# Kernel tuning notes

Measured on AMD Instinct MI355X. Metric: run time of the kernel, lower is better.

## Reference

```python
import jax, jax.numpy as jnp
import numpy as np

N = 100000
E = 1600000
FEAT = 128
EMBED = 128
CLASSES = 40


def _sage_conv(x, src, dst, W_l, W_r, b, n_nodes):
    # PyG SAGEConv (mean aggr): out = mean_{j in N(i)} x_j @ W_l + x_i @ W_r + b
    msg = x[src]                                                  # [E, d] gather
    agg = jax.ops.segment_sum(msg, dst, num_segments=n_nodes)     # [N, d]
    cnt = jax.ops.segment_sum(jnp.ones((src.shape[0], 1), x.dtype), dst,
                              num_segments=n_nodes)               # [N, 1]
    agg = agg / jnp.maximum(cnt, 1.0)                             # mean (0 for isolated)
    return agg @ W_l + x @ W_r + b


def setup_inputs() -> dict:
    key = jax.random.key(0)
    ks = jax.random.split(key, 10)
    s = lambda d: 1.0 / np.sqrt(d)
    x = jax.random.normal(ks[0], (N, FEAT), dtype=jnp.float32)
    edge_index = jax.random.randint(ks[1], (2, E), 0, N, dtype=jnp.int64)
    W1_l = jax.random.uniform(ks[2], (FEAT, EMBED), jnp.float32, -s(FEAT), s(FEAT))
    W1_r = jax.random.uniform(ks[3], (FEAT, EMBED), jnp.float32, -s(FEAT), s(FEAT))
    b1 = jnp.zeros((EMBED,), jnp.float32)
    W2_l = jax.random.uniform(ks[4], (EMBED, EMBED), jnp.float32, -s(EMBED), s(EMBED))
    W2_r = jax.random.uniform(ks[5], (EMBED, EMBED), jnp.float32, -s(EMBED), s(EMBED))
    b2 = jnp.zeros((EMBED,), jnp.float32)
    W_out = jax.random.uniform(ks[6], (EMBED, CLASSES), jnp.float32, -s(EMBED), s(EMBED))
    b_out = jax.random.uniform(ks[7], (CLASSES,), jnp.float32, -s(EMBED), s(EMBED))
    return {"x": x, "edge_index": edge_index,
            "W1_l": W1_l, "W1_r": W1_r, "b1": b1,
            "W2_l": W2_l, "W2_r": W2_r, "b2": b2,
            "W_out": W_out, "b_out": b_out}


def reference(x, edge_index, W1_l, W1_r, b1, W2_l, W2_r, b2, W_out, b_out):
    src, dst = edge_index[0], edge_index[1]
    n = x.shape[0]
    h = _sage_conv(x, src, dst, W1_l, W1_r, b1, n)   # [N, EMBED]
    h = _sage_conv(h, src, dst, W2_l, W2_r, b2, n)   # [N, EMBED]
    g = jnp.mean(h, axis=0, keepdims=True)           # global_mean_pool, batch=None -> [1, EMBED]
    return g @ W_out + b_out                          # [1, CLASSES]
```

## Files before the change

### kernel.cpp

```cpp
#include <hip/hip_runtime.h>


#define NN    100000
#define NE    1600000
#define FEAT  128
#define NCLS  40
#define NR    16
#define RSIZE 6250
#define NC    16
#define PER   (NE / 4 / NC)
#define FSB   2048


__global__ __launch_bounds__(1024) void k_cnt16(const int4* __restrict__ dst4, int* __restrict__ partial) {
    __shared__ int tab[RSIZE];
    const int c = blockIdx.x, r = blockIdx.y;
    for (int j = threadIdx.x; j < RSIZE; j += 1024) tab[j] = 0;
    __syncthreads();
    const int base = r * RSIZE;
    const int i0 = c * PER;
    for (int i = i0 + (int)threadIdx.x; i < i0 + PER; i += 1024) {
        int4 d = dst4[i];
        unsigned a;
        a = (unsigned)(d.x - base); if (a < RSIZE) atomicAdd(&tab[a], 1);
        a = (unsigned)(d.y - base); if (a < RSIZE) atomicAdd(&tab[a], 1);
        a = (unsigned)(d.z - base); if (a < RSIZE) atomicAdd(&tab[a], 1);
        a = (unsigned)(d.w - base); if (a < RSIZE) atomicAdd(&tab[a], 1);
    }
    __syncthreads();
    int* out = partial + (size_t)(r * NC + c) * RSIZE;
    for (int j = threadIdx.x; j < RSIZE; j += 1024) out[j] = tab[j];
}

__global__ __launch_bounds__(1024) void k_scat16(const int4* __restrict__ src4, const int4* __restrict__ dst4,
                                                 const float* __restrict__ val, float* __restrict__ partial) {
    __shared__ float tab[RSIZE];
    const int c = blockIdx.x, r = blockIdx.y;
    for (int j = threadIdx.x; j < RSIZE; j += 1024) tab[j] = 0.f;
    __syncthreads();
    const int base = r * RSIZE;
    const int i0 = c * PER;
    for (int i = i0 + (int)threadIdx.x; i < i0 + PER; i += 1024) {
        int4 s = src4[i];
        int4 d = dst4[i];
        unsigned a;
        a = (unsigned)(s.x - base); if (a < RSIZE) atomicAdd(&tab[a], val[d.x]);
        a = (unsigned)(s.y - base); if (a < RSIZE) atomicAdd(&tab[a], val[d.y]);
        a = (unsigned)(s.z - base); if (a < RSIZE) atomicAdd(&tab[a], val[d.z]);
        a = (unsigned)(s.w - base); if (a < RSIZE) atomicAdd(&tab[a], val[d.w]);
    }
    __syncthreads();
    float* out = partial + (size_t)(r * NC + c) * RSIZE;
    for (int j = threadIdx.x; j < RSIZE; j += 1024) out[j] = tab[j];
}

__global__ __launch_bounds__(256) void k_merge_invc(const int* __restrict__ partial, float* __restrict__ invc) {
    int i = blockIdx.x * 256 + threadIdx.x;
    if (i >= NN) return;
    int r = i / RSIZE, j = i - r * RSIZE;
    const int* p = partial + (size_t)r * NC * RSIZE + j;
    int cn = 0;
    #pragma unroll
    for (int c = 0; c < NC; ++c) cn += p[(size_t)c * RSIZE];
    invc[i] = 1.0f / (float)(cn > 0 ? cn : 1);
}

__global__ __launch_bounds__(256) void k_merge_ws(const float* __restrict__ partial, const float* __restrict__ invc,
                                                  float* __restrict__ ws, float* __restrict__ u) {
    int i = blockIdx.x * 256 + threadIdx.x;
    if (i >= NN) return;
    int r = i / RSIZE, j = i - r * RSIZE;
    const float* p = partial + (size_t)r * NC * RSIZE + j;
    float w = 0.f;
    #pragma unroll
    for (int c = 0; c < NC; ++c) w += p[(size_t)c * RSIZE];
    ws[i] = w;
    u[i] = w * invc[i];
}

__global__ __launch_bounds__(256) void k_merge_t(const float* __restrict__ partial, float* __restrict__ t) {
    int i = blockIdx.x * 256 + threadIdx.x;
    if (i >= NN) return;
    int r = i / RSIZE, j = i - r * RSIZE;
    const float* p = partial + (size_t)r * NC * RSIZE + j;
    float v = 0.f;
    #pragma unroll
    for (int c = 0; c < NC; ++c) v += p[(size_t)c * RSIZE];
    t[i] = v;
}


__global__ __launch_bounds__(256) void k_fs1(const float* __restrict__ x,
                                             const float* __restrict__ ws,
                                             const float* __restrict__ t,
                                             float* __restrict__ p1) {
    int lane = threadIdx.x & 31;
    int grp  = threadIdx.x >> 5;
    int row0 = blockIdx.x * 8 + grp;
    const int rstride = FSB * 8;

    float sx0=0,sx1=0,sx2=0,sx3=0;
    float sw0=0,sw1=0,sw2=0,sw3=0;
    float st0=0,st1=0,st2=0,st3=0;
    float wsum = 0.f;

    for (int r = row0; r < NN; r += rstride) {
        const float4* xr = (const float4*)(x + (size_t)r * FEAT);
        float4 v = xr[lane];
        float wr = ws[r];
        float tr = t[r];
        sx0 += v.x; sx1 += v.y; sx2 += v.z; sx3 += v.w;
        sw0 += wr*v.x; sw1 += wr*v.y; sw2 += wr*v.z; sw3 += wr*v.w;
        st0 += tr*v.x; st1 += tr*v.y; st2 += tr*v.z; st3 += tr*v.w;
        if (lane == 0) wsum += wr;
    }

    __shared__ float shx[8][32][4];
    __shared__ float shw[8][32][4];
    __shared__ float sht[8][32][4];
    __shared__ float shwsum[8];
    shx[grp][lane][0]=sx0; shx[grp][lane][1]=sx1; shx[grp][lane][2]=sx2; shx[grp][lane][3]=sx3;
    shw[grp][lane][0]=sw0; shw[grp][lane][1]=sw1; shw[grp][lane][2]=sw2; shw[grp][lane][3]=sw3;
    sht[grp][lane][0]=st0; sht[grp][lane][1]=st1; sht[grp][lane][2]=st2; sht[grp][lane][3]=st3;
    if (lane == 0) shwsum[grp] = wsum;
    __syncthreads();

    if (grp == 0) {
        const int b = blockIdx.x;
        float ax[4], aw[4], at[4];
        #pragma unroll
        for (int c = 0; c < 4; ++c) { ax[c]=shx[0][lane][c]; aw[c]=shw[0][lane][c]; at[c]=sht[0][lane][c]; }
        #pragma unroll
        for (int g = 1; g < 8; ++g) {
            #pragma unroll
            for (int c = 0; c < 4; ++c) {
                ax[c]+=shx[g][lane][c]; aw[c]+=shw[g][lane][c]; at[c]+=sht[g][lane][c];
            }
        }
        #pragma unroll
        for (int c = 0; c < 4; ++c) {
            p1[(size_t)(        4*lane + c) * FSB + b] = ax[c];
            p1[(size_t)(FEAT  + 4*lane + c) * FSB + b] = aw[c];
            p1[(size_t)(2*FEAT+ 4*lane + c) * FSB + b] = at[c];
        }
        if (lane == 0) {
            float w = shwsum[0];
            #pragma unroll
            for (int g = 1; g < 8; ++g) w += shwsum[g];
            p1[(size_t)(3*FEAT) * FSB + b] = w;
        }
    }
}

__global__ __launch_bounds__(256) void k_fs2(const float* __restrict__ p1, float* __restrict__ sums) {
    const int v = blockIdx.x;
    float s = 0.f;
    for (int b = threadIdx.x; b < FSB; b += 256) s += p1[(size_t)v * FSB + b];
    __shared__ float sh[256];
    sh[threadIdx.x] = s;
    __syncthreads();
    for (int off = 128; off > 0; off >>= 1) {
        if (threadIdx.x < off) sh[threadIdx.x] += sh[threadIdx.x + off];
        __syncthreads();
    }
    if (threadIdx.x == 0) sums[v] = sh[0];
}


__global__ __launch_bounds__(256) void k_count_dev(const int4* __restrict__ dst4, int* __restrict__ cnt) {
    int i = blockIdx.x * 256 + threadIdx.x;
    if (i >= NE / 4) return;
    int4 d = dst4[i];
    atomicAdd(&cnt[d.x], 1); atomicAdd(&cnt[d.y], 1);
    atomicAdd(&cnt[d.z], 1); atomicAdd(&cnt[d.w], 1);
}

__global__ __launch_bounds__(256) void k_inv_dev(const int* __restrict__ cnt, float* __restrict__ invc) {
    int i = blockIdx.x * 256 + threadIdx.x;
    if (i >= NN) return;
    int c = cnt[i];
    invc[i] = 1.0f / (float)(c > 0 ? c : 1);
}

__global__ __launch_bounds__(256) void k_ws_dev(const int4* __restrict__ src4, const int4* __restrict__ dst4,
                                                const float* __restrict__ invc, float* __restrict__ ws) {
    int i = blockIdx.x * 256 + threadIdx.x;
    if (i >= NE / 4) return;
    int4 s = src4[i];
    int4 d = dst4[i];
    atomicAdd(&ws[s.x], invc[d.x]); atomicAdd(&ws[s.y], invc[d.y]);
    atomicAdd(&ws[s.z], invc[d.z]); atomicAdd(&ws[s.w], invc[d.w]);
}

__global__ __launch_bounds__(256) void k_u_dev(const float* __restrict__ ws, const float* __restrict__ invc,
                                               float* __restrict__ u) {
    int i = blockIdx.x * 256 + threadIdx.x;
    if (i >= NN) return;
    u[i] = ws[i] * invc[i];
}

__global__ __launch_bounds__(256) void k_t_dev(const int4* __restrict__ src4, const int4* __restrict__ dst4,
                                               const float* __restrict__ u, float* __restrict__ t) {
    int i = blockIdx.x * 256 + threadIdx.x;
    if (i >= NE / 4) return;
    int4 s = src4[i];
    int4 d = dst4[i];
    atomicAdd(&t[s.x], u[d.x]); atomicAdd(&t[s.y], u[d.y]);
    atomicAdd(&t[s.z], u[d.z]); atomicAdd(&t[s.w], u[d.w]);
}

__global__ __launch_bounds__(256) void k_fs_atom(const float* __restrict__ x,
                                                 const float* __restrict__ ws,
                                                 const float* __restrict__ t,
                                                 float* __restrict__ sums) {
    int lane = threadIdx.x & 31;
    int grp  = threadIdx.x >> 5;
    int row0 = blockIdx.x * 8 + grp;
    int rstride = gridDim.x * 8;
    float sx0=0,sx1=0,sx2=0,sx3=0, sw0=0,sw1=0,sw2=0,sw3=0, st0=0,st1=0,st2=0,st3=0, wsum=0.f;
    for (int r = row0; r < NN; r += rstride) {
        const float4* xr = (const float4*)(x + (size_t)r * FEAT);
        float4 v = xr[lane];
        float wr = ws[r], tr = t[r];
        sx0+=v.x; sx1+=v.y; sx2+=v.z; sx3+=v.w;
        sw0+=wr*v.x; sw1+=wr*v.y; sw2+=wr*v.z; sw3+=wr*v.w;
        st0+=tr*v.x; st1+=tr*v.y; st2+=tr*v.z; st3+=tr*v.w;
        if (lane==0) wsum += wr;
    }
    __shared__ float shx[8][32][4], shw[8][32][4], sht[8][32][4], shwsum[8];
    shx[grp][lane][0]=sx0; shx[grp][lane][1]=sx1; shx[grp][lane][2]=sx2; shx[grp][lane][3]=sx3;
    shw[grp][lane][0]=sw0; shw[grp][lane][1]=sw1; shw[grp][lane][2]=sw2; shw[grp][lane][3]=sw3;
    sht[grp][lane][0]=st0; sht[grp][lane][1]=st1; sht[grp][lane][2]=st2; sht[grp][lane][3]=st3;
    if (lane==0) shwsum[grp]=wsum;
    __syncthreads();
    if (grp==0) {
        float ax[4], aw[4], at[4];
        #pragma unroll
        for (int c=0;c<4;++c){ax[c]=shx[0][lane][c];aw[c]=shw[0][lane][c];at[c]=sht[0][lane][c];}
        #pragma unroll
        for (int g=1;g<8;++g)
            #pragma unroll
            for (int c=0;c<4;++c){ax[c]+=shx[g][lane][c];aw[c]+=shw[g][lane][c];at[c]+=sht[g][lane][c];}
        #pragma unroll
        for (int c=0;c<4;++c){
            atomicAdd(&sums[        4*lane+c], ax[c]);
            atomicAdd(&sums[FEAT  + 4*lane+c], aw[c]);
            atomicAdd(&sums[2*FEAT+ 4*lane+c], at[c]);
        }
        if (lane==0){
            float w=shwsum[0];
            #pragma unroll
            for (int g=1;g<8;++g) w+=shwsum[g];
            atomicAdd(&sums[3*FEAT], w);
        }
    }
}


__global__ __launch_bounds__(128) void k_final(const float* __restrict__ sums,
                                               const float* __restrict__ W1l, const float* __restrict__ W1r,
                                               const float* __restrict__ b1,
                                               const float* __restrict__ W2l, const float* __restrict__ W2r,
                                               const float* __restrict__ b2,
                                               const float* __restrict__ Wout, const float* __restrict__ bout,
                                               float* __restrict__ out) {
    __shared__ float Sx[FEAT], Sw[FEAT], St[FEAT], M1[FEAT], S2[FEAT], G[FEAT];
    __shared__ float Wsum;
    int f = threadIdx.x;
    Sx[f] = sums[f];
    Sw[f] = sums[FEAT + f];
    St[f] = sums[2*FEAT + f];
    if (f == 0) Wsum = sums[3*FEAT];
    __syncthreads();

    float m1 = (float)NN * b1[f];
    float s2 = Wsum * b1[f];
    for (int k = 0; k < FEAT; ++k) {
        float wl = W1l[k*FEAT + f];
        float wr = W1r[k*FEAT + f];
        m1 += Sw[k]*wl + Sx[k]*wr;
        s2 += St[k]*wl + Sw[k]*wr;
    }
    M1[f] = m1; S2[f] = s2;
    __syncthreads();

    float g = 0.f;
    for (int k = 0; k < FEAT; ++k)
        g += S2[k]*W2l[k*FEAT + f] + M1[k]*W2r[k*FEAT + f];
    g = g * (1.0f/(float)NN) + b2[f];
    G[f] = g;
    __syncthreads();

    if (f < NCLS) {
        float o = bout[f];
        for (int k = 0; k < FEAT; ++k)
            o += G[k]*Wout[k*NCLS + f];
        out[f] = o;
    }
}


extern "C" void kernel_launch(void* const* d_in, const int* in_sizes, int n_in,
                              void* d_out, int out_size, void* d_ws, size_t ws_size,
                              hipStream_t stream) {
    const float* x    = (const float*)d_in[0];
    const int*   ei   = (const int*)d_in[1];
    const float* W1l  = (const float*)d_in[2];
    const float* W1r  = (const float*)d_in[3];
    const float* b1   = (const float*)d_in[4];
    const float* W2l  = (const float*)d_in[5];
    const float* W2r  = (const float*)d_in[6];
    const float* b2   = (const float*)d_in[7];
    const float* Wout = (const float*)d_in[8];
    const float* bout = (const float*)d_in[9];
    float* out = (float*)d_out;

    const int4* src4 = (const int4*)ei;
    const int4* dst4 = (const int4*)(ei + NE);

    const size_t need_lds = ((size_t)NR * NC * RSIZE + 640 + (size_t)4 * NN) * 4;

    if (ws_size >= need_lds) {
        float* partial = (float*)d_ws;
        size_t po = (size_t)NR * NC * RSIZE;
        float* sums = (float*)d_ws + po;
        float* invc = (float*)d_ws + po + 640;
        float* ws   = (float*)d_ws + po + 640 + (size_t)NN;
        float* u    = (float*)d_ws + po + 640 + (size_t)2*NN;
        float* t    = (float*)d_ws + po + 640 + (size_t)3*NN;
        float* p1   = partial;

        dim3 eg(NC, NR);
        const int NB = (NN + 255) / 256;

        k_cnt16<<<eg, 1024, 0, stream>>>(dst4, (int*)partial);
        k_merge_invc<<<NB, 256, 0, stream>>>((const int*)partial, invc);
        k_scat16<<<eg, 1024, 0, stream>>>(src4, dst4, invc, partial);
        k_merge_ws<<<NB, 256, 0, stream>>>(partial, invc, ws, u);
        k_scat16<<<eg, 1024, 0, stream>>>(src4, dst4, u, partial);
        k_merge_t<<<NB, 256, 0, stream>>>(partial, t);
        k_fs1<<<FSB, 256, 0, stream>>>(x, ws, t, p1);
        k_fs2<<<385, 256, 0, stream>>>(p1, sums);
        k_final<<<1, 128, 0, stream>>>(sums, W1l, W1r, b1, W2l, W2r, b2, Wout, bout, out);
    } else {
        int*   cnt  = (int*)d_ws;
        float* wsv  = (float*)d_ws + NN;
        float* t    = (float*)d_ws + 2*NN;
        float* sums = (float*)d_ws + 3*NN;
        float* invc = (float*)d_ws + 3*NN + 640;
        float* u    = (float*)d_ws + 3*NN + 640 + NN;

        hipMemsetAsync(d_ws, 0, ((size_t)3*NN + 640) * 4, stream);

        const int EB4 = (NE/4 + 255) / 256;
        const int NB  = (NN + 255) / 256;
        k_count_dev<<<EB4, 256, 0, stream>>>(dst4, cnt);
        k_inv_dev<<<NB, 256, 0, stream>>>(cnt, invc);
        k_ws_dev<<<EB4, 256, 0, stream>>>(src4, dst4, invc, wsv);
        k_u_dev<<<NB, 256, 0, stream>>>(wsv, invc, u);
        k_t_dev<<<EB4, 256, 0, stream>>>(src4, dst4, u, t);
        k_fs_atom<<<256, 256, 0, stream>>>(x, wsv, t, sums);
        k_final<<<1, 128, 0, stream>>>(sums, W1l, W1r, b1, W2l, W2r, b2, Wout, bout, out);
    }
}
```

Measured before the change: 205.7 us.

## Pack degree counts as 16-bit pairs and widen LDS range partitions

The degree-count histogram now packs two 16-bit counters per 32-bit LDS word, so each block covers twice as many nodes and fewer range passes over the edge list are needed. The scatter kernels use larger LDS tables (14336 floats) with 7 range slices and 64 edge chunks instead of 16x16, which cuts redundant re-reads of the edge arrays and raises the block count. The 16-bit counters assume no per-chunk count overflows 65535, and the larger partial buffers add merge traffic and need more workspace.

```diff
diff --git a/kernel.cpp b/kernel.cpp
--- a/kernel.cpp
+++ b/kernel.cpp
@@ -5,87 +5,106 @@
 #define NE    1600000
 #define FEAT  128
 #define NCLS  40
-#define NR    16
-#define RSIZE 6250
-#define NC    16
-#define PER   (NE / 4 / NC)
 #define FSB   2048
 
-
-__global__ __launch_bounds__(1024) void k_cnt16(const int4* __restrict__ dst4, int* __restrict__ partial) {
-    __shared__ int tab[RSIZE];
+#define B_RS   14336
+#define B_NR   7
+#define B_RSC  28672
+#define B_NRC  4
+#define B_NC   64
+
+#define S_RS   6250
+#define S_NR   16
+#define S_RSC  12500
+#define S_NRC  8
+#define S_NC   16
+
+
+template<int RSC, int NRC, int NCv>
+__global__ __launch_bounds__(1024) void k_cnt_p(const int4* __restrict__ dst4,
+                                                unsigned* __restrict__ partial) {
+    __shared__ unsigned tab[RSC / 2];
     const int c = blockIdx.x, r = blockIdx.y;
-    for (int j = threadIdx.x; j < RSIZE; j += 1024) tab[j] = 0;
-    __syncthreads();
-    const int base = r * RSIZE;
-    const int i0 = c * PER;
-    for (int i = i0 + (int)threadIdx.x; i < i0 + PER; i += 1024) {
+    for (int j = threadIdx.x; j < RSC / 2; j += 1024) tab[j] = 0u;
+    __syncthreads();
+    const int base = r * RSC;
+    const int PERv = (NE / 4) / NCv;
+    const int i0 = c * PERv;
+    for (int i = i0 + (int)threadIdx.x; i < i0 + PERv; i += 1024) {
         int4 d = dst4[i];
         unsigned a;
-        a = (unsigned)(d.x - base); if (a < RSIZE) atomicAdd(&tab[a], 1);
-        a = (unsigned)(d.y - base); if (a < RSIZE) atomicAdd(&tab[a], 1);
-        a = (unsigned)(d.z - base); if (a < RSIZE) atomicAdd(&tab[a], 1);
-        a = (unsigned)(d.w - base); if (a < RSIZE) atomicAdd(&tab[a], 1);
-    }
-    __syncthreads();
-    int* out = partial + (size_t)(r * NC + c) * RSIZE;
-    for (int j = threadIdx.x; j < RSIZE; j += 1024) out[j] = tab[j];
-}
-
-__global__ __launch_bounds__(1024) void k_scat16(const int4* __restrict__ src4, const int4* __restrict__ dst4,
-                                                 const float* __restrict__ val, float* __restrict__ partial) {
-    __shared__ float tab[RSIZE];
+        a = (unsigned)(d.x - base); if (a < RSC) atomicAdd(&tab[a >> 1], 1u << ((a & 1) * 16));
+        a = (unsigned)(d.y - base); if (a < RSC) atomicAdd(&tab[a >> 1], 1u << ((a & 1) * 16));
+        a = (unsigned)(d.z - base); if (a < RSC) atomicAdd(&tab[a >> 1], 1u << ((a & 1) * 16));
+        a = (unsigned)(d.w - base); if (a < RSC) atomicAdd(&tab[a >> 1], 1u << ((a & 1) * 16));
+    }
+    __syncthreads();
+    unsigned* out = partial + (size_t)(r * NCv + c) * (RSC / 2);
+    for (int j = threadIdx.x; j < RSC / 2; j += 1024) out[j] = tab[j];
+}
+
+template<int RS, int NRv, int NCv>
+__global__ __launch_bounds__(1024) void k_scat(const int4* __restrict__ src4, const int4* __restrict__ dst4,
+                                               const float* __restrict__ val, float* __restrict__ partial) {
+    __shared__ float tab[RS];
     const int c = blockIdx.x, r = blockIdx.y;
-    for (int j = threadIdx.x; j < RSIZE; j += 1024) tab[j] = 0.f;
-    __syncthreads();
-    const int base = r * RSIZE;
-    const int i0 = c * PER;
-    for (int i = i0 + (int)threadIdx.x; i < i0 + PER; i += 1024) {
+    for (int j = threadIdx.x; j < RS; j += 1024) tab[j] = 0.f;
+    __syncthreads();
+    const int base = r * RS;
+    const int PERv = (NE / 4) / NCv;
+    const int i0 = c * PERv;
+    for (int i = i0 + (int)threadIdx.x; i < i0 + PERv; i += 1024) {
         int4 s = src4[i];
         int4 d = dst4[i];
         unsigned a;
-        a = (unsigned)(s.x - base); if (a < RSIZE) atomicAdd(&tab[a], val[d.x]);
-        a = (unsigned)(s.y - base); if (a < RSIZE) atomicAdd(&tab[a], val[d.y]);
-        a = (unsigned)(s.z - base); if (a < RSIZE) atomicAdd(&tab[a], val[d.z]);
-        a = (unsigned)(s.w - base); if (a < RSIZE) atomicAdd(&tab[a], val[d.w]);
-    }
-    __syncthreads();
-    float* out = partial + (size_t)(r * NC + c) * RSIZE;
-    for (int j = threadIdx.x; j < RSIZE; j += 1024) out[j] = tab[j];
-}
-
-__global__ __launch_bounds__(256) void k_merge_invc(const int* __restrict__ partial, float* __restrict__ invc) {
+        a = (unsigned)(s.x - base); if (a < RS) atomicAdd(&tab[a], val[d.x]);
+        a = (unsigned)(s.y - base); if (a < RS) atomicAdd(&tab[a], val[d.y]);
+        a = (unsigned)(s.z - base); if (a < RS) atomicAdd(&tab[a], val[d.z]);
+        a = (unsigned)(s.w - base); if (a < RS) atomicAdd(&tab[a], val[d.w]);
+    }
+    __syncthreads();
+    float* out = partial + (size_t)(r * NCv + c) * RS;
+    for (int j = threadIdx.x; j < RS; j += 1024) out[j] = tab[j];
+}
+
+template<int RSC, int NRC, int NCv>
+__global__ __launch_bounds__(256) void k_merge_invc(const unsigned* __restrict__ partial,
+                                                    float* __restrict__ invc) {
     int i = blockIdx.x * 256 + threadIdx.x;
     if (i >= NN) return;
-    int r = i / RSIZE, j = i - r * RSIZE;
-    const int* p = partial + (size_t)r * NC * RSIZE + j;
+    int r = i / RSC, j = i - r * RSC;
+    const unsigned* p = partial + (size_t)r * NCv * (RSC / 2) + (j >> 1);
+    const unsigned sh = (unsigned)(j & 1) * 16u;
     int cn = 0;
     #pragma unroll
-    for (int c = 0; c < NC; ++c) cn += p[(size_t)c * RSIZE];
+    for (int c = 0; c < NCv; ++c) cn += (int)((p[(size_t)c * (RSC / 2)] >> sh) & 0xFFFFu);
     invc[i] = 1.0f / (float)(cn > 0 ? cn : 1);
 }
 
-__global__ __launch_bounds__(256) void k_merge_ws(const float* __restrict__ partial, const float* __restrict__ invc,
+template<int RS, int NRv, int NCv>
+__global__ __launch_bounds__(256) void k_merge_ws(const float* __restrict__ partial,
+                                                  const float* __restrict__ invc,
                                                   float* __restrict__ ws, float* __restrict__ u) {
     int i = blockIdx.x * 256 + threadIdx.x;
     if (i >= NN) return;
-    int r = i / RSIZE, j = i - r * RSIZE;
-    const float* p = partial + (size_t)r * NC * RSIZE + j;
+    int r = i / RS, j = i - r * RS;
+    const float* p = partial + (size_t)r * NCv * RS + j;
     float w = 0.f;
     #pragma unroll
-    for (int c = 0; c < NC; ++c) w += p[(size_t)c * RSIZE];
+    for (int c = 0; c < NCv; ++c) w += p[(size_t)c * RS];
     ws[i] = w;
     u[i] = w * invc[i];
 }
 
+template<int RS, int NRv, int NCv>
 __global__ __launch_bounds__(256) void k_merge_t(const float* __restrict__ partial, float* __restrict__ t) {
     int i = blockIdx.x * 256 + threadIdx.x;
     if (i >= NN) return;
-    int r = i / RSIZE, j = i - r * RSIZE;
-    const float* p = partial + (size_t)r * NC * RSIZE + j;
+    int r = i / RS, j = i - r * RS;
+    const float* p = partial + (size_t)r * NCv * RS + j;
     float v = 0.f;
     #pragma unroll
-    for (int c = 0; c < NC; ++c) v += p[(size_t)c * RSIZE];
+    for (int c = 0; c < NCv; ++c) v += p[(size_t)c * RS];
     t[i] = v;
 }
 
@@ -300,6 +319,36 @@
 }
 
 
+template<int RS, int NRv, int RSC, int NRC, int NCv>
+static void run_cfg(const float* x, const int4* src4, const int4* dst4,
+                    const float* W1l, const float* W1r, const float* b1,
+                    const float* W2l, const float* W2r, const float* b2,
+                    const float* Wout, const float* bout,
+                    float* out, void* d_ws, hipStream_t stream) {
+    const size_t scat_par = (size_t)NRv * NCv * RS;
+    float* partial = (float*)d_ws;
+    float* sums = (float*)d_ws + scat_par;
+    float* invc = (float*)d_ws + scat_par + 640;
+    float* ws   = (float*)d_ws + scat_par + 640 + (size_t)NN;
+    float* u    = (float*)d_ws + scat_par + 640 + (size_t)2*NN;
+    float* t    = (float*)d_ws + scat_par + 640 + (size_t)3*NN;
+    float* p1   = partial;
+
+    const int NB = (NN + 255) / 256;
+    dim3 gc(NCv, NRC);
+    dim3 gs(NCv, NRv);
+
+    k_cnt_p<RSC, NRC, NCv><<<gc, 1024, 0, stream>>>(dst4, (unsigned*)partial);
+    k_merge_invc<RSC, NRC, NCv><<<NB, 256, 0, stream>>>((const unsigned*)partial, invc);
+    k_scat<RS, NRv, NCv><<<gs, 1024, 0, stream>>>(src4, dst4, invc, partial);
+    k_merge_ws<RS, NRv, NCv><<<NB, 256, 0, stream>>>(partial, invc, ws, u);
+    k_scat<RS, NRv, NCv><<<gs, 1024, 0, stream>>>(src4, dst4, u, partial);
+    k_merge_t<RS, NRv, NCv><<<NB, 256, 0, stream>>>(partial, t);
+    k_fs1<<<FSB, 256, 0, stream>>>(x, ws, t, p1);
+    k_fs2<<<385, 256, 0, stream>>>(p1, sums);
+    k_final<<<1, 128, 0, stream>>>(sums, W1l, W1r, b1, W2l, W2r, b2, Wout, bout, out);
+}
+
 extern "C" void kernel_launch(void* const* d_in, const int* in_sizes, int n_in,
                               void* d_out, int out_size, void* d_ws, size_t ws_size,
                               hipStream_t stream) {
@@ -318,30 +367,16 @@
     const int4* src4 = (const int4*)ei;
     const int4* dst4 = (const int4*)(ei + NE);
 
-    const size_t need_lds = ((size_t)NR * NC * RSIZE + 640 + (size_t)4 * NN) * 4;
-
-    if (ws_size >= need_lds) {
-        float* partial = (float*)d_ws;
-        size_t po = (size_t)NR * NC * RSIZE;
-        float* sums = (float*)d_ws + po;
-        float* invc = (float*)d_ws + po + 640;
-        float* ws   = (float*)d_ws + po + 640 + (size_t)NN;
-        float* u    = (float*)d_ws + po + 640 + (size_t)2*NN;
-        float* t    = (float*)d_ws + po + 640 + (size_t)3*NN;
-        float* p1   = partial;
-
-        dim3 eg(NC, NR);
-        const int NB = (NN + 255) / 256;
-
-        k_cnt16<<<eg, 1024, 0, stream>>>(dst4, (int*)partial);
-        k_merge_invc<<<NB, 256, 0, stream>>>((const int*)partial, invc);
-        k_scat16<<<eg, 1024, 0, stream>>>(src4, dst4, invc, partial);
-        k_merge_ws<<<NB, 256, 0, stream>>>(partial, invc, ws, u);
-        k_scat16<<<eg, 1024, 0, stream>>>(src4, dst4, u, partial);
-        k_merge_t<<<NB, 256, 0, stream>>>(partial, t);
-        k_fs1<<<FSB, 256, 0, stream>>>(x, ws, t, p1);
-        k_fs2<<<385, 256, 0, stream>>>(p1, sums);
-        k_final<<<1, 128, 0, stream>>>(sums, W1l, W1r, b1, W2l, W2r, b2, Wout, bout, out);
+    auto need = [](size_t scat_par) { return (scat_par + 640 + (size_t)4 * NN) * 4; };
+    const size_t big_par   = (size_t)B_NR * B_NC * B_RS;
+    const size_t small_par = (size_t)S_NR * S_NC * S_RS;
+
+    if (ws_size >= need(big_par)) {
+        run_cfg<B_RS, B_NR, B_RSC, B_NRC, B_NC>(x, src4, dst4, W1l, W1r, b1, W2l, W2r, b2,
+                                                Wout, bout, out, d_ws, stream);
+    } else if (ws_size >= need(small_par)) {
+        run_cfg<S_RS, S_NR, S_RSC, S_NRC, S_NC>(x, src4, dst4, W1l, W1r, b1, W2l, W2r, b2,
+                                                Wout, bout, out, d_ws, stream);
     } else {
         int*   cnt  = (int*)d_ws;
         float* wsv  = (float*)d_ws + NN;
```

Result: slower. 221.9 us (+7.9%).

## Fuse all stages into one cooperative persistent kernel with grid syncs

Applied to the files above, without the earlier changes.

Replaces nine separate kernel launches (count, merges, two scatters, feature sums, final GEMV) with a single cooperative kernel of 256 blocks of 1024 threads, using grid.sync between phases and a union of shared-memory tables. This removes per-launch overhead and inter-kernel gaps. In exchange it adds grid-wide barriers, the final reduction runs on one block only, and the path needs cooperative-launch support with every block co-resident.

```diff
diff --git a/kernel.cpp b/kernel.cpp
--- a/kernel.cpp
+++ b/kernel.cpp
@@ -1,4 +1,7 @@
 #include <hip/hip_runtime.h>
+#include <hip/hip_cooperative_groups.h>
+
+namespace cg = cooperative_groups;
 
 
 #define NN    100000
@@ -6,164 +9,223 @@
 #define FEAT  128
 #define NCLS  40
 #define NR    16
-#define RSIZE 6250
+#define RS    6250
 #define NC    16
-#define PER   (NE / 4 / NC)
-#define FSB   2048
-
-
-__global__ __launch_bounds__(1024) void k_cnt16(const int4* __restrict__ dst4, int* __restrict__ partial) {
-    __shared__ int tab[RSIZE];
-    const int c = blockIdx.x, r = blockIdx.y;
-    for (int j = threadIdx.x; j < RSIZE; j += 1024) tab[j] = 0;
-    __syncthreads();
-    const int base = r * RSIZE;
+#define PER   25000
+#define GRID  256
+#define BLK   1024
+
+struct FS {
+    float shx[32][32][4];
+    float shw[32][32][4];
+    float sht[32][32][4];
+    float wsum[32];
+};
+union SH {
+    unsigned ctab[RS];
+    float    ftab[RS];
+    FS       fs;
+    float    fin[800];
+};
+
+__global__ __launch_bounds__(BLK, 4) void k_all(
+        const float* __restrict__ x,
+        const int4* __restrict__ src4, const int4* __restrict__ dst4,
+        const float* __restrict__ W1l, const float* __restrict__ W1r, const float* __restrict__ b1,
+        const float* __restrict__ W2l, const float* __restrict__ W2r, const float* __restrict__ b2,
+        const float* __restrict__ Wout, const float* __restrict__ bout,
+        float* __restrict__ out,
+        float* __restrict__ partial, float* __restrict__ invc,
+        float* __restrict__ ws, float* __restrict__ u, float* __restrict__ t,
+        float* __restrict__ fsbuf) {
+    cg::grid_group grid = cg::this_grid();
+    __shared__ SH sh;
+
+    const int bid = blockIdx.x;
+    const int tid = threadIdx.x;
+    const int c = bid & (NC - 1);
+    const int r = bid >> 4;
+    const int base = r * RS;
     const int i0 = c * PER;
-    for (int i = i0 + (int)threadIdx.x; i < i0 + PER; i += 1024) {
+
+    for (int j = tid; j < RS; j += BLK) sh.ctab[j] = 0u;
+    __syncthreads();
+    for (int i = i0 + tid; i < i0 + PER; i += BLK) {
         int4 d = dst4[i];
         unsigned a;
-        a = (unsigned)(d.x - base); if (a < RSIZE) atomicAdd(&tab[a], 1);
-        a = (unsigned)(d.y - base); if (a < RSIZE) atomicAdd(&tab[a], 1);
-        a = (unsigned)(d.z - base); if (a < RSIZE) atomicAdd(&tab[a], 1);
-        a = (unsigned)(d.w - base); if (a < RSIZE) atomicAdd(&tab[a], 1);
-    }
-    __syncthreads();
-    int* out = partial + (size_t)(r * NC + c) * RSIZE;
-    for (int j = threadIdx.x; j < RSIZE; j += 1024) out[j] = tab[j];
-}
-
-__global__ __launch_bounds__(1024) void k_scat16(const int4* __restrict__ src4, const int4* __restrict__ dst4,
-                                                 const float* __restrict__ val, float* __restrict__ partial) {
-    __shared__ float tab[RSIZE];
-    const int c = blockIdx.x, r = blockIdx.y;
-    for (int j = threadIdx.x; j < RSIZE; j += 1024) tab[j] = 0.f;
-    __syncthreads();
-    const int base = r * RSIZE;
-    const int i0 = c * PER;
-    for (int i = i0 + (int)threadIdx.x; i < i0 + PER; i += 1024) {
+        a = (unsigned)(d.x - base); if (a < RS) atomicAdd(&sh.ctab[a], 1u);
+        a = (unsigned)(d.y - base); if (a < RS) atomicAdd(&sh.ctab[a], 1u);
+        a = (unsigned)(d.z - base); if (a < RS) atomicAdd(&sh.ctab[a], 1u);
+        a = (unsigned)(d.w - base); if (a < RS) atomicAdd(&sh.ctab[a], 1u);
+    }
+    __syncthreads();
+    {
+        unsigned* outp = (unsigned*)partial + (size_t)(r * NC + c) * RS;
+        for (int j = tid; j < RS; j += BLK) outp[j] = sh.ctab[j];
+    }
+    grid.sync();
+
+    {
+        int i = bid * BLK + tid;
+        if (i < NN) {
+            int rr = i / RS, jj = i - rr * RS;
+            const unsigned* p = (const unsigned*)partial + (size_t)rr * NC * RS + jj;
+            unsigned cn = 0;
+            #pragma unroll
+            for (int cc = 0; cc < NC; ++cc) cn += p[(size_t)cc * RS];
+            invc[i] = 1.0f / (float)(cn > 0u ? cn : 1u);
+        }
+    }
+    grid.sync();
+
+    for (int j = tid; j < RS; j += BLK) sh.ftab[j] = 0.f;
+    __syncthreads();
+    for (int i = i0 + tid; i < i0 + PER; i += BLK) {
         int4 s = src4[i];
         int4 d = dst4[i];
         unsigned a;
-        a = (unsigned)(s.x - base); if (a < RSIZE) atomicAdd(&tab[a], val[d.x]);
-        a = (unsigned)(s.y - base); if (a < RSIZE) atomicAdd(&tab[a], val[d.y]);
-        a = (unsigned)(s.z - base); if (a < RSIZE) atomicAdd(&tab[a], val[d.z]);
-        a = (unsigned)(s.w - base); if (a < RSIZE) atomicAdd(&tab[a], val[d.w]);
-    }
-    __syncthreads();
-    float* out = partial + (size_t)(r * NC + c) * RSIZE;
-    for (int j = threadIdx.x; j < RSIZE; j += 1024) out[j] = tab[j];
-}
-
-__global__ __launch_bounds__(256) void k_merge_invc(const int* __restrict__ partial, float* __restrict__ invc) {
-    int i = blockIdx.x * 256 + threadIdx.x;
-    if (i >= NN) return;
-    int r = i / RSIZE, j = i - r * RSIZE;
-    const int* p = partial + (size_t)r * NC * RSIZE + j;
-    int cn = 0;
-    #pragma unroll
-    for (int c = 0; c < NC; ++c) cn += p[(size_t)c * RSIZE];
-    invc[i] = 1.0f / (float)(cn > 0 ? cn : 1);
-}
-
-__global__ __launch_bounds__(256) void k_merge_ws(const float* __restrict__ partial, const float* __restrict__ invc,
-                                                  float* __restrict__ ws, float* __restrict__ u) {
-    int i = blockIdx.x * 256 + threadIdx.x;
-    if (i >= NN) return;
-    int r = i / RSIZE, j = i - r * RSIZE;
-    const float* p = partial + (size_t)r * NC * RSIZE + j;
-    float w = 0.f;
-    #pragma unroll
-    for (int c = 0; c < NC; ++c) w += p[(size_t)c * RSIZE];
-    ws[i] = w;
-    u[i] = w * invc[i];
-}
-
-__global__ __launch_bounds__(256) void k_merge_t(const float* __restrict__ partial, float* __restrict__ t) {
-    int i = blockIdx.x * 256 + threadIdx.x;
-    if (i >= NN) return;
-    int r = i / RSIZE, j = i - r * RSIZE;
-    const float* p = partial + (size_t)r * NC * RSIZE + j;
-    float v = 0.f;
-    #pragma unroll
-    for (int c = 0; c < NC; ++c) v += p[(size_t)c * RSIZE];
-    t[i] = v;
-}
-
-
-__global__ __launch_bounds__(256) void k_fs1(const float* __restrict__ x,
-                                             const float* __restrict__ ws,
-                                             const float* __restrict__ t,
-                                             float* __restrict__ p1) {
-    int lane = threadIdx.x & 31;
-    int grp  = threadIdx.x >> 5;
-    int row0 = blockIdx.x * 8 + grp;
-    const int rstride = FSB * 8;
-
-    float sx0=0,sx1=0,sx2=0,sx3=0;
-    float sw0=0,sw1=0,sw2=0,sw3=0;
-    float st0=0,st1=0,st2=0,st3=0;
-    float wsum = 0.f;
-
-    for (int r = row0; r < NN; r += rstride) {
-        const float4* xr = (const float4*)(x + (size_t)r * FEAT);
-        float4 v = xr[lane];
-        float wr = ws[r];
-        float tr = t[r];
-        sx0 += v.x; sx1 += v.y; sx2 += v.z; sx3 += v.w;
-        sw0 += wr*v.x; sw1 += wr*v.y; sw2 += wr*v.z; sw3 += wr*v.w;
-        st0 += tr*v.x; st1 += tr*v.y; st2 += tr*v.z; st3 += tr*v.w;
-        if (lane == 0) wsum += wr;
-    }
-
-    __shared__ float shx[8][32][4];
-    __shared__ float shw[8][32][4];
-    __shared__ float sht[8][32][4];
-    __shared__ float shwsum[8];
-    shx[grp][lane][0]=sx0; shx[grp][lane][1]=sx1; shx[grp][lane][2]=sx2; shx[grp][lane][3]=sx3;
-    shw[grp][lane][0]=sw0; shw[grp][lane][1]=sw1; shw[grp][lane][2]=sw2; shw[grp][lane][3]=sw3;
-    sht[grp][lane][0]=st0; sht[grp][lane][1]=st1; sht[grp][lane][2]=st2; sht[grp][lane][3]=st3;
-    if (lane == 0) shwsum[grp] = wsum;
-    __syncthreads();
-
-    if (grp == 0) {
-        const int b = blockIdx.x;
-        float ax[4], aw[4], at[4];
-        #pragma unroll
-        for (int c = 0; c < 4; ++c) { ax[c]=shx[0][lane][c]; aw[c]=shw[0][lane][c]; at[c]=sht[0][lane][c]; }
-        #pragma unroll
-        for (int g = 1; g < 8; ++g) {
-            #pragma unroll
-            for (int c = 0; c < 4; ++c) {
-                ax[c]+=shx[g][lane][c]; aw[c]+=shw[g][lane][c]; at[c]+=sht[g][lane][c];
+        a = (unsigned)(s.x - base); if (a < RS) atomicAdd(&sh.ftab[a], invc[d.x]);
+        a = (unsigned)(s.y - base); if (a < RS) atomicAdd(&sh.ftab[a], invc[d.y]);
+        a = (unsigned)(s.z - base); if (a < RS) atomicAdd(&sh.ftab[a], invc[d.z]);
+        a = (unsigned)(s.w - base); if (a < RS) atomicAdd(&sh.ftab[a], invc[d.w]);
+    }
+    __syncthreads();
+    {
+        float* outp = partial + (size_t)(r * NC + c) * RS;
+        for (int j = tid; j < RS; j += BLK) outp[j] = sh.ftab[j];
+    }
+    grid.sync();
+
+    {
+        int i = bid * BLK + tid;
+        if (i < NN) {
+            int rr = i / RS, jj = i - rr * RS;
+            const float* p = partial + (size_t)rr * NC * RS + jj;
+            float w = 0.f;
+            #pragma unroll
+            for (int cc = 0; cc < NC; ++cc) w += p[(size_t)cc * RS];
+            ws[i] = w;
+            u[i] = w * invc[i];
+        }
+    }
+    grid.sync();
+
+    for (int j = tid; j < RS; j += BLK) sh.ftab[j] = 0.f;
+    __syncthreads();
+    for (int i = i0 + tid; i < i0 + PER; i += BLK) {
+        int4 s = src4[i];
+        int4 d = dst4[i];
+        unsigned a;
+        a = (unsigned)(s.x - base); if (a < RS) atomicAdd(&sh.ftab[a], u[d.x]);
+        a = (unsigned)(s.y - base); if (a < RS) atomicAdd(&sh.ftab[a], u[d.y]);
+        a = (unsigned)(s.z - base); if (a < RS) atomicAdd(&sh.ftab[a], u[d.z]);
+        a = (unsigned)(s.w - base); if (a < RS) atomicAdd(&sh.ftab[a], u[d.w]);
+    }
+    __syncthreads();
+    {
+        float* outp = partial + (size_t)(r * NC + c) * RS;
+        for (int j = tid; j < RS; j += BLK) outp[j] = sh.ftab[j];
+    }
+    grid.sync();
+
+    {
+        int i = bid * BLK + tid;
+        if (i < NN) {
+            int rr = i / RS, jj = i - rr * RS;
+            const float* p = partial + (size_t)rr * NC * RS + jj;
+            float v = 0.f;
+            #pragma unroll
+            for (int cc = 0; cc < NC; ++cc) v += p[(size_t)cc * RS];
+            t[i] = v;
+        }
+    }
+    grid.sync();
+
+    {
+        const int lane = tid & 31;
+        const int grp  = tid >> 5;
+        float sx0=0,sx1=0,sx2=0,sx3=0;
+        float sw0=0,sw1=0,sw2=0,sw3=0;
+        float st0=0,st1=0,st2=0,st3=0;
+        float wsum = 0.f;
+        for (int row = bid * 32 + grp; row < NN; row += GRID * 32) {
+            const float4* xr = (const float4*)(x + (size_t)row * FEAT);
+            float4 v = xr[lane];
+            float wr = ws[row];
+            float tr = t[row];
+            sx0 += v.x; sx1 += v.y; sx2 += v.z; sx3 += v.w;
+            sw0 += wr*v.x; sw1 += wr*v.y; sw2 += wr*v.z; sw3 += wr*v.w;
+            st0 += tr*v.x; st1 += tr*v.y; st2 += tr*v.z; st3 += tr*v.w;
+            if (lane == 0) wsum += wr;
+        }
+        __syncthreads();
+        sh.fs.shx[grp][lane][0]=sx0; sh.fs.shx[grp][lane][1]=sx1;
+        sh.fs.shx[grp][lane][2]=sx2; sh.fs.shx[grp][lane][3]=sx3;
+        sh.fs.shw[grp][lane][0]=sw0; sh.fs.shw[grp][lane][1]=sw1;
+        sh.fs.shw[grp][lane][2]=sw2; sh.fs.shw[grp][lane][3]=sw3;
+        sh.fs.sht[grp][lane][0]=st0; sh.fs.sht[grp][lane][1]=st1;
+        sh.fs.sht[grp][lane][2]=st2; sh.fs.sht[grp][lane][3]=st3;
+        if (lane == 0) sh.fs.wsum[grp] = wsum;
+        __syncthreads();
+        if (grp == 0) {
+            float ax[4]={0,0,0,0}, aw[4]={0,0,0,0}, at[4]={0,0,0,0};
+            for (int g = 0; g < 32; ++g) {
+                #pragma unroll
+                for (int cc = 0; cc < 4; ++cc) {
+                    ax[cc] += sh.fs.shx[g][lane][cc];
+                    aw[cc] += sh.fs.shw[g][lane][cc];
+                    at[cc] += sh.fs.sht[g][lane][cc];
+                }
             }
-        }
-        #pragma unroll
-        for (int c = 0; c < 4; ++c) {
-            p1[(size_t)(        4*lane + c) * FSB + b] = ax[c];
-            p1[(size_t)(FEAT  + 4*lane + c) * FSB + b] = aw[c];
-            p1[(size_t)(2*FEAT+ 4*lane + c) * FSB + b] = at[c];
-        }
-        if (lane == 0) {
-            float w = shwsum[0];
-            #pragma unroll
-            for (int g = 1; g < 8; ++g) w += shwsum[g];
-            p1[(size_t)(3*FEAT) * FSB + b] = w;
-        }
-    }
-}
-
-__global__ __launch_bounds__(256) void k_fs2(const float* __restrict__ p1, float* __restrict__ sums) {
-    const int v = blockIdx.x;
-    float s = 0.f;
-    for (int b = threadIdx.x; b < FSB; b += 256) s += p1[(size_t)v * FSB + b];
-    __shared__ float sh[256];
-    sh[threadIdx.x] = s;
-    __syncthreads();
-    for (int off = 128; off > 0; off >>= 1) {
-        if (threadIdx.x < off) sh[threadIdx.x] += sh[threadIdx.x + off];
-        __syncthreads();
-    }
-    if (threadIdx.x == 0) sums[v] = sh[0];
+            #pragma unroll
+            for (int cc = 0; cc < 4; ++cc) {
+                fsbuf[(size_t)(        4*lane + cc) * GRID + bid] = ax[cc];
+                fsbuf[(size_t)(FEAT  + 4*lane + cc) * GRID + bid] = aw[cc];
+                fsbuf[(size_t)(2*FEAT+ 4*lane + cc) * GRID + bid] = at[cc];
+            }
+            if (lane == 0) {
+                float w = 0.f;
+                for (int g = 0; g < 32; ++g) w += sh.fs.wsum[g];
+                fsbuf[(size_t)(3*FEAT) * GRID + bid] = w;
+            }
+        }
+    }
+    grid.sync();
+
+    if (bid != 0) return;
+    for (int v = tid; v < 3*FEAT + 1; v += BLK) {
+        const float* pp = fsbuf + (size_t)v * GRID;
+        float s = 0.f;
+        for (int b = 0; b < GRID; ++b) s += pp[b];
+        sh.fin[v] = s;
+    }
+    __syncthreads();
+    if (tid < FEAT) {
+        float m1 = (float)NN * b1[tid];
+        float s2 = sh.fin[384] * b1[tid];
+        for (int k = 0; k < FEAT; ++k) {
+            float wl = W1l[k*FEAT + tid];
+            float wr = W1r[k*FEAT + tid];
+            m1 += sh.fin[128 + k] * wl + sh.fin[k] * wr;
+            s2 += sh.fin[256 + k] * wl + sh.fin[128 + k] * wr;
+        }
+        sh.fin[400 + tid] = m1;
+        sh.fin[528 + tid] = s2;
+    }
+    __syncthreads();
+    if (tid < FEAT) {
+        float g = 0.f;
+        for (int k = 0; k < FEAT; ++k)
+            g += sh.fin[528 + k] * W2l[k*FEAT + tid] + sh.fin[400 + k] * W2r[k*FEAT + tid];
+        sh.fin[656 + tid] = g * (1.0f / (float)NN) + b2[tid];
+    }
+    __syncthreads();
+    if (tid < NCLS) {
+        float o = bout[tid];
+        for (int k = 0; k < FEAT; ++k)
+            o += sh.fin[656 + k] * Wout[k*NCLS + tid];
+        out[tid] = o;
+    }
 }
 
 
@@ -256,7 +318,6 @@
     }
 }
 
-
 __global__ __launch_bounds__(128) void k_final(const float* __restrict__ sums,
                                                const float* __restrict__ W1l, const float* __restrict__ W1r,
                                                const float* __restrict__ b1,
@@ -272,7 +333,6 @@
     St[f] = sums[2*FEAT + f];
     if (f == 0) Wsum = sums[3*FEAT];
     __syncthreads();
-
     float m1 = (float)NN * b1[f];
     float s2 = Wsum * b1[f];
     for (int k = 0; k < FEAT; ++k) {
@@ -283,14 +343,12 @@
     }
     M1[f] = m1; S2[f] = s2;
     __syncthreads();
-
     float g = 0.f;
     for (int k = 0; k < FEAT; ++k)
         g += S2[k]*W2l[k*FEAT + f] + M1[k]*W2r[k*FEAT + f];
     g = g * (1.0f/(float)NN) + b2[f];
     G[f] = g;
     __syncthreads();
-
     if (f < NCLS) {
         float o = bout[f];
         for (int k = 0; k < FEAT; ++k)
@@ -318,30 +376,28 @@
     const int4* src4 = (const int4*)ei;
     const int4* dst4 = (const int4*)(ei + NE);
 
-    const size_t need_lds = ((size_t)NR * NC * RSIZE + 640 + (size_t)4 * NN) * 4;
-
-    if (ws_size >= need_lds) {
+    int dev = 0, coop = 0;
+    hipGetDevice(&dev);
+    hipDeviceGetAttribute(&coop, hipDeviceAttributeCooperativeLaunch, dev);
+
+    const size_t need_coop = ((size_t)NR*NC*RS + 4*(size_t)NN + (size_t)(3*FEAT+1)*GRID) * 4;
+
+    if (coop && ws_size >= need_coop) {
         float* partial = (float*)d_ws;
-        size_t po = (size_t)NR * NC * RSIZE;
-        float* sums = (float*)d_ws + po;
-        float* invc = (float*)d_ws + po + 640;
-        float* ws   = (float*)d_ws + po + 640 + (size_t)NN;
-        float* u    = (float*)d_ws + po + 640 + (size_t)2*NN;
-        float* t    = (float*)d_ws + po + 640 + (size_t)3*NN;
-        float* p1   = partial;
-
-        dim3 eg(NC, NR);
-        const int NB = (NN + 255) / 256;
-
-        k_cnt16<<<eg, 1024, 0, stream>>>(dst4, (int*)partial);
-        k_merge_invc<<<NB, 256, 0, stream>>>((const int*)partial, invc);
-        k_scat16<<<eg, 1024, 0, stream>>>(src4, dst4, invc, partial);
-        k_merge_ws<<<NB, 256, 0, stream>>>(partial, invc, ws, u);
-        k_scat16<<<eg, 1024, 0, stream>>>(src4, dst4, u, partial);
-        k_merge_t<<<NB, 256, 0, stream>>>(partial, t);
-        k_fs1<<<FSB, 256, 0, stream>>>(x, ws, t, p1);
-        k_fs2<<<385, 256, 0, stream>>>(p1, sums);
-        k_final<<<1, 128, 0, stream>>>(sums, W1l, W1r, b1, W2l, W2r, b2, Wout, bout, out);
+        float* invc = partial + (size_t)NR*NC*RS;
+        float* ws   = invc + NN;
+        float* u    = ws + NN;
+        float* t    = u + NN;
+        float* fsb  = t + NN;
+
+        void* args[] = {
+            (void*)&x, (void*)&src4, (void*)&dst4,
+            (void*)&W1l, (void*)&W1r, (void*)&b1,
+            (void*)&W2l, (void*)&W2r, (void*)&b2,
+            (void*)&Wout, (void*)&bout, (void*)&out,
+            (void*)&partial, (void*)&invc, (void*)&ws, (void*)&u, (void*)&t, (void*)&fsb
+        };
+        hipLaunchCooperativeKernel((const void*)k_all, dim3(GRID), dim3(BLK), args, 0, stream);
     } else {
         int*   cnt  = (int*)d_ws;
         float* wsv  = (float*)d_ws + NN;
```

New measurement: 446.9 us. 117% more time.

## Widen LDS histogram ranges with packed 16-bit counters and fewer range passes

Applied to the files above, without the earlier changes.

The degree count now packs two 16-bit counters per LDS word, so each block covers 12500 nodes and only 8 range passes over the edge list are needed instead of 16. The float scatter kernels use 16000-entry LDS tables with 7 range passes and 32 edge chunks. Fewer range passes mean each edge is reread fewer times, which should cut redundant global edge traffic. The costs are larger per-block LDS use, which may lower occupancy, and 32-way partial merges instead of 16-way.

```diff
diff --git a/kernel.cpp b/kernel.cpp
--- a/kernel.cpp
+++ b/kernel.cpp
@@ -3,89 +3,104 @@
 
 #define NN    100000
 #define NE    1600000
+#define NE4   (NE/4)
 #define FEAT  128
 #define NCLS  40
-#define NR    16
-#define RSIZE 6250
-#define NC    16
-#define PER   (NE / 4 / NC)
 #define FSB   2048
 
-
-__global__ __launch_bounds__(1024) void k_cnt16(const int4* __restrict__ dst4, int* __restrict__ partial) {
-    __shared__ int tab[RSIZE];
+#define RSC   12500
+#define NRC   8
+#define NCC   32
+#define PERC  12500
+
+#define RSV   16000
+#define NRV   7
+#define NCV   32
+#define PERV  12500
+
+
+__global__ __launch_bounds__(1024) void k_cnt(const int4* __restrict__ dst4,
+                                              unsigned* __restrict__ pc) {
+    __shared__ unsigned tab[RSC / 2];
     const int c = blockIdx.x, r = blockIdx.y;
-    for (int j = threadIdx.x; j < RSIZE; j += 1024) tab[j] = 0;
-    __syncthreads();
-    const int base = r * RSIZE;
-    const int i0 = c * PER;
-    for (int i = i0 + (int)threadIdx.x; i < i0 + PER; i += 1024) {
+    for (int j = threadIdx.x; j < RSC / 2; j += 1024) tab[j] = 0u;
+    __syncthreads();
+    const int base = r * RSC;
+    const int i0 = c * PERC;
+    for (int i = i0 + (int)threadIdx.x; i < i0 + PERC; i += 1024) {
         int4 d = dst4[i];
         unsigned a;
-        a = (unsigned)(d.x - base); if (a < RSIZE) atomicAdd(&tab[a], 1);
-        a = (unsigned)(d.y - base); if (a < RSIZE) atomicAdd(&tab[a], 1);
-        a = (unsigned)(d.z - base); if (a < RSIZE) atomicAdd(&tab[a], 1);
-        a = (unsigned)(d.w - base); if (a < RSIZE) atomicAdd(&tab[a], 1);
-    }
-    __syncthreads();
-    int* out = partial + (size_t)(r * NC + c) * RSIZE;
-    for (int j = threadIdx.x; j < RSIZE; j += 1024) out[j] = tab[j];
-}
-
-__global__ __launch_bounds__(1024) void k_scat16(const int4* __restrict__ src4, const int4* __restrict__ dst4,
-                                                 const float* __restrict__ val, float* __restrict__ partial) {
-    __shared__ float tab[RSIZE];
+        a = (unsigned)(d.x - base); if (a < RSC) atomicAdd(&tab[a >> 1], 1u << ((a & 1) * 16));
+        a = (unsigned)(d.y - base); if (a < RSC) atomicAdd(&tab[a >> 1], 1u << ((a & 1) * 16));
+        a = (unsigned)(d.z - base); if (a < RSC) atomicAdd(&tab[a >> 1], 1u << ((a & 1) * 16));
+        a = (unsigned)(d.w - base); if (a < RSC) atomicAdd(&tab[a >> 1], 1u << ((a & 1) * 16));
+    }
+    __syncthreads();
+    unsigned* outp = pc + (size_t)(r * NCC + c) * (RSC / 2);
+    for (int j = threadIdx.x; j < RSC / 2; j += 1024) outp[j] = tab[j];
+}
+
+__global__ __launch_bounds__(256) void k_merge_invc(const unsigned* __restrict__ pc,
+                                                    float* __restrict__ invc) {
+    int i = blockIdx.x * 256 + threadIdx.x;
+    if (i >= NN) return;
+    int rr = i / RSC, jj = i - rr * RSC;
+    const unsigned* p = pc + (size_t)rr * NCC * (RSC / 2) + (jj >> 1);
+    const unsigned sh = (unsigned)(jj & 1) * 16u;
+    unsigned cn = 0;
+    #pragma unroll
+    for (int c = 0; c < NCC; ++c) cn += (p[(size_t)c * (RSC / 2)] >> sh) & 0xFFFFu;
+    invc[i] = 1.0f / (float)(cn > 0u ? cn : 1u);
+}
+
+
+__global__ __launch_bounds__(1024) void k_scat(const int4* __restrict__ src4,
+                                               const int4* __restrict__ dst4,
+                                               const float* __restrict__ val,
+                                               float* __restrict__ partial) {
+    __shared__ float tab[RSV];
     const int c = blockIdx.x, r = blockIdx.y;
-    for (int j = threadIdx.x; j < RSIZE; j += 1024) tab[j] = 0.f;
-    __syncthreads();
-    const int base = r * RSIZE;
-    const int i0 = c * PER;
-    for (int i = i0 + (int)threadIdx.x; i < i0 + PER; i += 1024) {
+    for (int j = threadIdx.x; j < RSV; j += 1024) tab[j] = 0.f;
+    __syncthreads();
+    const int base = r * RSV;
+    const int i0 = c * PERV;
+    for (int i = i0 + (int)threadIdx.x; i < i0 + PERV; i += 1024) {
         int4 s = src4[i];
         int4 d = dst4[i];
         unsigned a;
-        a = (unsigned)(s.x - base); if (a < RSIZE) atomicAdd(&tab[a], val[d.x]);
-        a = (unsigned)(s.y - base); if (a < RSIZE) atomicAdd(&tab[a], val[d.y]);
-        a = (unsigned)(s.z - base); if (a < RSIZE) atomicAdd(&tab[a], val[d.z]);
-        a = (unsigned)(s.w - base); if (a < RSIZE) atomicAdd(&tab[a], val[d.w]);
-    }
-    __syncthreads();
-    float* out = partial + (size_t)(r * NC + c) * RSIZE;
-    for (int j = threadIdx.x; j < RSIZE; j += 1024) out[j] = tab[j];
-}
-
-__global__ __launch_bounds__(256) void k_merge_invc(const int* __restrict__ partial, float* __restrict__ invc) {
-    int i = blockIdx.x * 256 + threadIdx.x;
-    if (i >= NN) return;
-    int r = i / RSIZE, j = i - r * RSIZE;
-    const int* p = partial + (size_t)r * NC * RSIZE + j;
-    int cn = 0;
-    #pragma unroll
-    for (int c = 0; c < NC; ++c) cn += p[(size_t)c * RSIZE];
-    invc[i] = 1.0f / (float)(cn > 0 ? cn : 1);
-}
-
-__global__ __launch_bounds__(256) void k_merge_ws(const float* __restrict__ partial, const float* __restrict__ invc,
+        a = (unsigned)(s.x - base); if (a < RSV) atomicAdd(&tab[a], val[d.x]);
+        a = (unsigned)(s.y - base); if (a < RSV) atomicAdd(&tab[a], val[d.y]);
+        a = (unsigned)(s.z - base); if (a < RSV) atomicAdd(&tab[a], val[d.z]);
+        a = (unsigned)(s.w - base); if (a < RSV) atomicAdd(&tab[a], val[d.w]);
+    }
+    __syncthreads();
+    float* outp = partial + (size_t)(r * NCV + c) * RSV;
+    for (int j = threadIdx.x; j < RSV; j += 1024) outp[j] = tab[j];
+}
+
+__global__ __launch_bounds__(256) void k_merge_ws(const float* __restrict__ partial,
+                                                  const float* __restrict__ invc,
                                                   float* __restrict__ ws, float* __restrict__ u) {
     int i = blockIdx.x * 256 + threadIdx.x;
     if (i >= NN) return;
-    int r = i / RSIZE, j = i - r * RSIZE;
-    const float* p = partial + (size_t)r * NC * RSIZE + j;
+    int rr = i / RSV, jj = i - rr * RSV;
+    const float* p = partial + (size_t)rr * NCV * RSV + jj;
     float w = 0.f;
     #pragma unroll
-    for (int c = 0; c < NC; ++c) w += p[(size_t)c * RSIZE];
+    for (int c = 0; c < NCV; ++c) w += p[(size_t)c * RSV];
     ws[i] = w;
     u[i] = w * invc[i];
 }
 
-__global__ __launch_bounds__(256) void k_merge_t(const float* __restrict__ partial, float* __restrict__ t) {
-    int i = blockIdx.x * 256 + threadIdx.x;
-    if (i >= NN) return;
-    int r = i / RSIZE, j = i - r * RSIZE;
-    const float* p = partial + (size_t)r * NC * RSIZE + j;
+__global__ __launch_bounds__(256) void k_merge_t(const float* __restrict__ partial,
+                                                 float* __restrict__ t) {
+    int i = blockIdx.x * 256 + threadIdx.x;
+    if (i >= NN) return;
+    int rr = i / RSV, jj = i - rr * RSV;
+    const float* p = partial + (size_t)rr * NCV * RSV + jj;
     float v = 0.f;
     #pragma unroll
-    for (int c = 0; c < NC; ++c) v += p[(size_t)c * RSIZE];
+    for (int c = 0; c < NCV; ++c) v += p[(size_t)c * RSV];
     t[i] = v;
 }
 
@@ -167,9 +182,52 @@
 }
 
 
+__global__ __launch_bounds__(128) void k_final(const float* __restrict__ sums,
+                                               const float* __restrict__ W1l, const float* __restrict__ W1r,
+                                               const float* __restrict__ b1,
+                                               const float* __restrict__ W2l, const float* __restrict__ W2r,
+                                               const float* __restrict__ b2,
+                                               const float* __restrict__ Wout, const float* __restrict__ bout,
+                                               float* __restrict__ out) {
+    __shared__ float Sx[FEAT], Sw[FEAT], St[FEAT], M1[FEAT], S2[FEAT], G[FEAT];
+    __shared__ float Wsum;
+    int f = threadIdx.x;
+    Sx[f] = sums[f];
+    Sw[f] = sums[FEAT + f];
+    St[f] = sums[2*FEAT + f];
+    if (f == 0) Wsum = sums[3*FEAT];
+    __syncthreads();
+
+    float m1 = (float)NN * b1[f];
+    float s2 = Wsum * b1[f];
+    for (int k = 0; k < FEAT; ++k) {
+        float wl = W1l[k*FEAT + f];
+        float wr = W1r[k*FEAT + f];
+        m1 += Sw[k]*wl + Sx[k]*wr;
+        s2 += St[k]*wl + Sw[k]*wr;
+    }
+    M1[f] = m1; S2[f] = s2;
+    __syncthreads();
+
+    float g = 0.f;
+    for (int k = 0; k < FEAT; ++k)
+        g += S2[k]*W2l[k*FEAT + f] + M1[k]*W2r[k*FEAT + f];
+    g = g * (1.0f/(float)NN) + b2[f];
+    G[f] = g;
+    __syncthreads();
+
+    if (f < NCLS) {
+        float o = bout[f];
+        for (int k = 0; k < FEAT; ++k)
+            o += G[k]*Wout[k*NCLS + f];
+        out[f] = o;
+    }
+}
+
+
 __global__ __launch_bounds__(256) void k_count_dev(const int4* __restrict__ dst4, int* __restrict__ cnt) {
     int i = blockIdx.x * 256 + threadIdx.x;
-    if (i >= NE / 4) return;
+    if (i >= NE4) return;
     int4 d = dst4[i];
     atomicAdd(&cnt[d.x], 1); atomicAdd(&cnt[d.y], 1);
     atomicAdd(&cnt[d.z], 1); atomicAdd(&cnt[d.w], 1);
@@ -185,7 +243,7 @@
 __global__ __launch_bounds__(256) void k_ws_dev(const int4* __restrict__ src4, const int4* __restrict__ dst4,
                                                 const float* __restrict__ invc, float* __restrict__ ws) {
     int i = blockIdx.x * 256 + threadIdx.x;
-    if (i >= NE / 4) return;
+    if (i >= NE4) return;
     int4 s = src4[i];
     int4 d = dst4[i];
     atomicAdd(&ws[s.x], invc[d.x]); atomicAdd(&ws[s.y], invc[d.y]);
@@ -202,7 +260,7 @@
 __global__ __launch_bounds__(256) void k_t_dev(const int4* __restrict__ src4, const int4* __restrict__ dst4,
                                                const float* __restrict__ u, float* __restrict__ t) {
     int i = blockIdx.x * 256 + threadIdx.x;
-    if (i >= NE / 4) return;
+    if (i >= NE4) return;
     int4 s = src4[i];
     int4 d = dst4[i];
     atomicAdd(&t[s.x], u[d.x]); atomicAdd(&t[s.y], u[d.y]);
@@ -257,49 +315,6 @@
 }
 
 
-__global__ __launch_bounds__(128) void k_final(const float* __restrict__ sums,
-                                               const float* __restrict__ W1l, const float* __restrict__ W1r,
-                                               const float* __restrict__ b1,
-                                               const float* __restrict__ W2l, const float* __restrict__ W2r,
-                                               const float* __restrict__ b2,
-                                               const float* __restrict__ Wout, const float* __restrict__ bout,
-                                               float* __restrict__ out) {
-    __shared__ float Sx[FEAT], Sw[FEAT], St[FEAT], M1[FEAT], S2[FEAT], G[FEAT];
-    __shared__ float Wsum;
-    int f = threadIdx.x;
-    Sx[f] = sums[f];
-    Sw[f] = sums[FEAT + f];
-    St[f] = sums[2*FEAT + f];
-    if (f == 0) Wsum = sums[3*FEAT];
-    __syncthreads();
-
-    float m1 = (float)NN * b1[f];
-    float s2 = Wsum * b1[f];
-    for (int k = 0; k < FEAT; ++k) {
-        float wl = W1l[k*FEAT + f];
-        float wr = W1r[k*FEAT + f];
-        m1 += Sw[k]*wl + Sx[k]*wr;
-        s2 += St[k]*wl + Sw[k]*wr;
-    }
-    M1[f] = m1; S2[f] = s2;
-    __syncthreads();
-
-    float g = 0.f;
-    for (int k = 0; k < FEAT; ++k)
-        g += S2[k]*W2l[k*FEAT + f] + M1[k]*W2r[k*FEAT + f];
-    g = g * (1.0f/(float)NN) + b2[f];
-    G[f] = g;
-    __syncthreads();
-
-    if (f < NCLS) {
-        float o = bout[f];
-        for (int k = 0; k < FEAT; ++k)
-            o += G[k]*Wout[k*NCLS + f];
-        out[f] = o;
-    }
-}
-
-
 extern "C" void kernel_launch(void* const* d_in, const int* in_sizes, int n_in,
                               void* d_out, int out_size, void* d_ws, size_t ws_size,
                               hipStream_t stream) {
@@ -318,29 +333,27 @@
     const int4* src4 = (const int4*)ei;
     const int4* dst4 = (const int4*)(ei + NE);
 
-    const size_t need_lds = ((size_t)NR * NC * RSIZE + 640 + (size_t)4 * NN) * 4;
-
-    if (ws_size >= need_lds) {
+    const size_t PART = (size_t)NRV * NCV * RSV;
+    const size_t need = (PART + (size_t)4*NN + 640) * 4;
+
+    if (ws_size >= need) {
         float* partial = (float*)d_ws;
-        size_t po = (size_t)NR * NC * RSIZE;
-        float* sums = (float*)d_ws + po;
-        float* invc = (float*)d_ws + po + 640;
-        float* ws   = (float*)d_ws + po + 640 + (size_t)NN;
-        float* u    = (float*)d_ws + po + 640 + (size_t)2*NN;
-        float* t    = (float*)d_ws + po + 640 + (size_t)3*NN;
-        float* p1   = partial;
-
-        dim3 eg(NC, NR);
+        float* invc = partial + PART;
+        float* ws   = invc + NN;
+        float* u    = ws + NN;
+        float* t    = u + NN;
+        float* sums = t + NN;
+
         const int NB = (NN + 255) / 256;
 
-        k_cnt16<<<eg, 1024, 0, stream>>>(dst4, (int*)partial);
-        k_merge_invc<<<NB, 256, 0, stream>>>((const int*)partial, invc);
-        k_scat16<<<eg, 1024, 0, stream>>>(src4, dst4, invc, partial);
+        k_cnt<<<dim3(NCC, NRC), 1024, 0, stream>>>(dst4, (unsigned*)partial);
+        k_merge_invc<<<NB, 256, 0, stream>>>((const unsigned*)partial, invc);
+        k_scat<<<dim3(NCV, NRV), 1024, 0, stream>>>(src4, dst4, invc, partial);
         k_merge_ws<<<NB, 256, 0, stream>>>(partial, invc, ws, u);
-        k_scat16<<<eg, 1024, 0, stream>>>(src4, dst4, u, partial);
+        k_scat<<<dim3(NCV, NRV), 1024, 0, stream>>>(src4, dst4, u, partial);
         k_merge_t<<<NB, 256, 0, stream>>>(partial, t);
-        k_fs1<<<FSB, 256, 0, stream>>>(x, ws, t, p1);
-        k_fs2<<<385, 256, 0, stream>>>(p1, sums);
+        k_fs1<<<FSB, 256, 0, stream>>>(x, ws, t, partial);
+        k_fs2<<<385, 256, 0, stream>>>(partial, sums);
         k_final<<<1, 128, 0, stream>>>(sums, W1l, W1r, b1, W2l, W2r, b2, Wout, bout, out);
     } else {
         int*   cnt  = (int*)d_ws;
@@ -352,7 +365,7 @@
 
         hipMemsetAsync(d_ws, 0, ((size_t)3*NN + 640) * 4, stream);
 
-        const int EB4 = (NE/4 + 255) / 256;
+        const int EB4 = (NE4 + 255) / 256;
         const int NB  = (NN + 255) / 256;
         k_count_dev<<<EB4, 256, 0, stream>>>(dst4, cnt);
         k_inv_dev<<<NB, 256, 0, stream>>>(cnt, invc);
```

New measurement: 189.9 us. 1.08x faster.
